# Kernel optimization log

Hardware: AMD Instinct MI355X
Metric: run time of the kernel (lower is better)

Reference implementation:

```python
import jax, jax.numpy as jnp
import numpy as np

SPACE_DIM = 3
D = SPACE_DIM + 1            # (t, x, y, z)
D_MODEL = 1024
N_LAYERS = 4                 # hidden layers
N_MIX = 64
TRI = D * (D - 1) // 2       # strict upper-triangular entries of A
OUT_DIM = N_MIX * (TRI + 1)  # per-mixture triu values + mixture logits
TRIU_I, TRIU_J = np.triu_indices(D, k=1)
RHO_SCALE = 10.0


def setup_inputs() -> dict:
    key = jax.random.key(0)
    ks = jax.random.split(key, 8)
    B = 65536
    x = jax.random.normal(ks[0], (B, D), jnp.float32)
    W0 = jax.random.normal(ks[1], (D, D_MODEL), jnp.float32) * np.float32(np.sqrt(2.0 / D))
    b0 = jnp.zeros((D_MODEL,), jnp.float32)
    Wh = jax.random.normal(ks[2], (N_LAYERS, D_MODEL, D_MODEL), jnp.float32) * np.float32(np.sqrt(2.0 / D_MODEL))
    bh = jnp.zeros((N_LAYERS, D_MODEL), jnp.float32)
    Wout = jax.random.normal(ks[3], (D_MODEL, OUT_DIM), jnp.float32) * np.float32(np.sqrt(1.0 / D_MODEL))
    bout = jnp.zeros((OUT_DIM,), jnp.float32)
    return dict(x=x, W0=W0, b0=b0, Wh=Wh, bh=bh, Wout=Wout, bout=bout)


def _mlp(z, W0, b0, Wh, bh, Wout, bout):
    # z: (D,) -> (OUT_DIM,), swish MLP (NeuralConservationLaw backbone)
    h = jax.nn.silu(z @ W0 + b0)
    for l in range(N_LAYERS):  # fixed small layer count: python loop ok
        h = jax.nn.silu(h @ Wh[l] + bh[l])
    return h @ Wout + bout


def _A(z, params):
    # Antisymmetric matrix field A(z): mixture-weighted strict-upper-tri values.
    out = _mlp(z, *params)                              # (OUT_DIM,)
    logits = out[:N_MIX]                                # (N_MIX,)
    vals = out[N_MIX:].reshape(N_MIX, TRI)              # (N_MIX, TRI)
    a = jax.nn.softmax(logits) @ vals                   # (TRI,)
    A = jnp.zeros((D, D), out.dtype).at[TRIU_I, TRIU_J].set(a)
    return A - A.T                                      # antisymmetric (D, D)


def reference(x, W0, b0, Wh, bh, Wout, bout):
    params = (W0, b0, Wh, bh, Wout, bout)

    def u_single(z):
        # u_i = sum_j dA_ij/dz_j  (row-divergence of antisymmetric A => div u = 0)
        J = jax.jacfwd(lambda zz: _A(zz, params))(z)    # (D, D, D): J[i,j,k]=dA_ij/dz_k
        return jnp.einsum('ijj->i', J)                  # (D,)

    u = jax.vmap(u_single)(x)                           # (B, D)
    rho = u[..., :1] * RHO_SCALE
    flux = u[..., 1:]
    return jnp.concatenate([rho, flux], axis=-1)
```

## Files before the change

### kernel.cpp

```cpp
#include <hip/hip_runtime.h>
#include <hip/hip_bf16.h>

typedef _Float16 half8 __attribute__((ext_vector_type(8)));
typedef _Float16 half4 __attribute__((ext_vector_type(4)));
typedef float floatx4 __attribute__((ext_vector_type(4)));

__device__ __forceinline__ float bfu2f(unsigned short u) {
  return __uint_as_float(((unsigned)u) << 16);
}

__device__ __forceinline__ void gld16(const void* g, void* l) {
  __builtin_amdgcn_global_load_lds((const __attribute__((address_space(1))) void*)g,
                                   (__attribute__((address_space(3))) void*)l, 16, 0, 0);
}

__device__ __forceinline__ float fast_sig(float v) {
  return __builtin_amdgcn_rcpf(1.f + __expf(-v));
}

template <int NC>
__device__ __forceinline__ void xcd_decode(int lin, int NR, int& r, int& c) {
  if (NR & 7) {
    c = lin % NC;
    r = lin / NC;
  } else {
    int rl = lin & 7;
    int t = lin >> 3;
    c = t % NC;
    r = (t / NC) * 8 + rl;
  }
}

__global__ void probe_kernel(const unsigned short* __restrict__ w0, int* __restrict__ flag) {
  __shared__ int s;
  if (threadIdx.x == 0) s = 0;
  __syncthreads();
  int big = 0;
  for (int i = threadIdx.x; i < 2048; i += 256) {
    unsigned e = (w0[i] >> 7) & 0xFFu;
    if (e >= 134u) big = 1;
  }
  if (big) atomicOr(&s, 1);
  __syncthreads();
  if (threadIdx.x == 0) *flag = s;
}

__global__ void cvt_kernel(const void* __restrict__ in, _Float16* __restrict__ out, int nOut,
                           int nIn, const int* __restrict__ flag) {
  int i = blockIdx.x * 256 + threadIdx.x;
  if (i >= nOut) return;
  float v = 0.f;
  if (i < nIn) v = (*flag) ? ((const float*)in)[i] : bfu2f(((const unsigned short*)in)[i]);
  out[i] = (_Float16)v;
}

__global__ void tr_kernel(const void* __restrict__ in, _Float16* __restrict__ out, int Nin,
                          long inStride, long outStride, const int* __restrict__ flag) {
  __shared__ float tile[32][33];
  const int f = *flag;
  int k0 = blockIdx.x * 32, n0 = blockIdx.y * 32;
  long ib = (long)blockIdx.z * inStride;
  long ob = (long)blockIdx.z * outStride;
  int tx = threadIdx.x, ty = threadIdx.y;
#pragma unroll
  for (int i = 0; i < 4; i++) {
    int k = k0 + ty + i * 8, n = n0 + tx;
    float v = 0.f;
    if (n < Nin) {
      long idx = ib + (long)k * Nin + n;
      v = f ? ((const float*)in)[idx] : bfu2f(((const unsigned short*)in)[idx]);
    }
    tile[ty + i * 8][tx] = v;
  }
  __syncthreads();
#pragma unroll
  for (int i = 0; i < 4; i++) {
    int n = n0 + ty + i * 8, k = k0 + tx;
    out[ob + (long)n * 1024 + k] = (_Float16)tile[tx][ty + i * 8];
  }
}

__global__ __launch_bounds__(256)
void layer0_kernel(const _Float16* __restrict__ x16, const _Float16* __restrict__ W0c,
                   const _Float16* __restrict__ b0c, _Float16* __restrict__ H,
                   int chunkBase, int S1) {
  const int lb = blockIdx.x;
  const int t = threadIdx.x;
  const long gb = (long)chunkBase + lb;
  float z0 = (float)x16[gb * 4 + 0];
  float z1 = (float)x16[gb * 4 + 1];
  float z2 = (float)x16[gb * 4 + 2];
  float z3 = (float)x16[gb * 4 + 3];
  const int j0 = t * 4;
  float w[4][4];
#pragma unroll
  for (int i = 0; i < 4; i++) {
    half4 wv = *(const half4*)&W0c[i * 1024 + j0];
#pragma unroll
    for (int jj = 0; jj < 4; jj++) w[i][jj] = (float)wv[jj];
  }
  half4 o[5];
#pragma unroll
  for (int jj = 0; jj < 4; jj++) {
    float pre = z0 * w[0][jj] + z1 * w[1][jj] + z2 * w[2][jj] + z3 * w[3][jj] +
                (float)b0c[j0 + jj];
    float s = fast_sig(pre);
    o[0][jj] = (_Float16)(pre * s);
    float ds = s * (1.f + pre * (1.f - s));
    o[1][jj] = (_Float16)(ds * w[0][jj]);
    o[2][jj] = (_Float16)(ds * w[1][jj]);
    o[3][jj] = (_Float16)(ds * w[2][jj]);
    o[4][jj] = (_Float16)(ds * w[3][jj]);
  }
  long rowbase = (long)lb * 1024 + j0;
#pragma unroll
  for (int s = 0; s < 5; s++) *(half4*)&H[(long)s * S1 + rowbase] = o[s];
}

__global__ __launch_bounds__(256, 3)
void gemm_h1(const _Float16* __restrict__ A, const _Float16* __restrict__ Bt,
             const _Float16* __restrict__ bias, _Float16* __restrict__ C,
             _Float16* __restrict__ DS, int NR) {
  constexpr int K = 1024;
  __shared__ _Float16 SM[8192];
  _Float16* As = SM;
  _Float16* Bs = SM + 4096;
  _Float16* Ep = SM;
  const int tid = threadIdx.x;
  const int wave = tid >> 6;
  const int lane = tid & 63;
  int rb, cb;
  xcd_decode<8>(blockIdx.x, NR, rb, cb);
  const int n0 = cb * 128;
  const long m0 = (long)rb * 128;

  const int srow0 = (wave * 2 + 0) * 16 + (lane >> 2);
  const int srow1 = (wave * 2 + 1) * 16 + (lane >> 2);
  const int scol = (lane & 3) * 8;
  const _Float16* gA0 = A + (m0 + srow0) * K + scol;
  const _Float16* gA1 = A + (m0 + srow1) * K + scol;
  const _Float16* gB0 = Bt + (long)(n0 + srow0) * K + scol;
  const _Float16* gB1 = Bt + (long)(n0 + srow1) * K + scol;
  _Float16* lA0 = As + (wave * 2 + 0) * 512;
  _Float16* lA1 = As + (wave * 2 + 1) * 512;
  _Float16* lB0 = Bs + (wave * 2 + 0) * 512;
  _Float16* lB1 = Bs + (wave * 2 + 1) * 512;

  const int wm = (wave & 1) * 64;
  const int wn = (wave >> 1) * 64;
  const int fr = lane & 15;
  const int fc = (lane >> 4) * 8;
  const int c0f = lane & 15;
  const int rqk = lane >> 4;
  const int myRound = wave & 1;

  float bv[4];
#pragma unroll
  for (int ni = 0; ni < 4; ni++) bv[ni] = (float)bias[n0 + wn + ni * 16 + c0f];

  const int erow = tid >> 4;
  const int ecol = (tid & 15) * 8;
  const int ecolp = ecol ^ (wave << 4);

  floatx4 acc[4][4];
#pragma unroll
  for (int i = 0; i < 4; i++)
#pragma unroll
    for (int j = 0; j < 4; j++) acc[i][j] = (floatx4)(0.f);

  for (int kk = 0; kk < K; kk += 32) {
    __syncthreads();
    gld16(gA0 + kk, lA0);
    gld16(gA1 + kk, lA1);
    gld16(gB0 + kk, lB0);
    gld16(gB1 + kk, lB1);
    __syncthreads();
    half8 af[4], bf[4];
#pragma unroll
    for (int i = 0; i < 4; i++) af[i] = *(const half8*)&As[(wm + i * 16 + fr) * 32 + fc];
#pragma unroll
    for (int i = 0; i < 4; i++) bf[i] = *(const half8*)&Bs[(wn + i * 16 + fr) * 32 + fc];
#pragma unroll
    for (int mi = 0; mi < 4; mi++)
#pragma unroll
      for (int ni = 0; ni < 4; ni++)
        acc[mi][ni] = __builtin_amdgcn_mfma_f32_16x16x32_f16(af[mi], bf[ni], acc[mi][ni], 0, 0, 0);
  }

#pragma unroll
  for (int r = 0; r < 2; r++) {
    __syncthreads();
    if (myRound == r) {
#pragma unroll
      for (int mi = 0; mi < 4; mi++)
#pragma unroll
        for (int ni = 0; ni < 4; ni++) {
          int colp = (wn + ni * 16 + c0f) ^ (rqk << 4);
#pragma unroll
          for (int rr = 0; rr < 4; rr++) {
            int row_local = mi * 16 + rqk * 4 + rr;
            Ep[row_local * 128 + colp] = (_Float16)(acc[mi][ni][rr] + bv[ni]);
          }
        }
    }
    __syncthreads();
#pragma unroll
    for (int p = 0; p < 4; p++) {
      int row_local = p * 16 + erow;
      half8 vv = *(const half8*)&Ep[row_local * 128 + ecolp];
      long row = m0 + r * 64 + row_local;
      half8 hv, dv;
#pragma unroll
      for (int e = 0; e < 8; e++) {
        float xv = (float)vv[e];
        float sg = fast_sig(xv);
        hv[e] = (_Float16)(xv * sg);
        dv[e] = (_Float16)(sg * (1.f + xv * (1.f - sg)));
      }
      *(half8*)&C[row * (long)K + n0 + ecol] = hv;
      *(half8*)&DS[row * (long)K + n0 + ecol] = dv;
    }
  }
}

__global__ __launch_bounds__(512, 2)
void gemm_h2(const _Float16* __restrict__ A, const _Float16* __restrict__ Bt,
             _Float16* __restrict__ C, const _Float16* __restrict__ DS, int bcMask, int NR) {
  constexpr int K = 1024;
  __shared__ _Float16 SM[49152];
  const int tid = threadIdx.x;
  const int wave = tid >> 6;
  const int lane = tid & 63;
  int rb, cb;
  xcd_decode<4>(blockIdx.x, NR, rb, cb);
  const long m0 = (long)rb * 256;
  const int n0 = cb * 256;

  const int srow = wave * 32 + (lane >> 2);
  const int scol = ((lane & 3) ^ ((lane >> 3) & 3)) * 8;
  const _Float16* gA0 = A + (m0 + srow) * K + scol;
  const _Float16* gA1 = gA0 + 16 * K;
  const _Float16* gB0 = Bt + (long)(n0 + srow) * K + scol;
  const _Float16* gB1 = gB0 + 16 * K;
  const int loff0 = wave * 1024;
  const int loff1 = loff0 + 512;

  const int wr = wave >> 2;
  const int wc = wave & 3;
  const int fr = lane & 15;
  const int fc = ((lane >> 4) ^ ((lane >> 1) & 3)) * 8;
  const int rqk = lane >> 4;
  const int c0f = lane & 15;

  floatx4 acc[8][4];
#pragma unroll
  for (int i = 0; i < 8; i++)
#pragma unroll
    for (int j = 0; j < 4; j++) acc[i][j] = (floatx4)(0.f);

  {
    _Float16* b0p = SM;
    gld16(gA0 + 0, b0p + loff0);
    gld16(gA1 + 0, b0p + loff1);
    gld16(gB0 + 0, b0p + 8192 + loff0);
    gld16(gB1 + 0, b0p + 8192 + loff1);
    _Float16* b1p = SM + 16384;
    gld16(gA0 + 32, b1p + loff0);
    gld16(gA1 + 32, b1p + loff1);
    gld16(gB0 + 32, b1p + 8192 + loff0);
    gld16(gB1 + 32, b1p + 8192 + loff1);
  }

  int bufCur = 0;
  int bufNxt = 2;
  for (int it = 0; it < 32; ++it) {
    if (it < 31) __builtin_amdgcn_s_waitcnt(0x0F74);
    else         __builtin_amdgcn_s_waitcnt(0x0F70);
    __builtin_amdgcn_s_barrier();
    const int kk = (it + 2) * 32;
    _Float16* bp = SM + bufNxt * 16384;
    if (it < 30) {
      gld16(gA0 + kk, bp + loff0);
      gld16(gA1 + kk, bp + loff1);
    }
    const _Float16* Asb = SM + bufCur * 16384;
    const _Float16* Bsb = Asb + 8192;
    half8 af[8], bf0, bf1, bf2, bf3;
#pragma unroll
    for (int i = 0; i < 8; i++)
      af[i] = *(const half8*)&Asb[(wr * 128 + i * 16 + fr) * 32 + fc];
    bf0 = *(const half8*)&Bsb[(wc * 64 + 0 * 16 + fr) * 32 + fc];
    bf1 = *(const half8*)&Bsb[(wc * 64 + 1 * 16 + fr) * 32 + fc];
    __builtin_amdgcn_s_setprio(1);
#pragma unroll
    for (int mi = 0; mi < 8; mi++) {
      acc[mi][0] = __builtin_amdgcn_mfma_f32_16x16x32_f16(af[mi], bf0, acc[mi][0], 0, 0, 0);
      acc[mi][1] = __builtin_amdgcn_mfma_f32_16x16x32_f16(af[mi], bf1, acc[mi][1], 0, 0, 0);
    }
    __builtin_amdgcn_s_setprio(0);
    if (it < 30) {
      gld16(gB0 + kk, bp + 8192 + loff0);
      gld16(gB1 + kk, bp + 8192 + loff1);
    }
    bf2 = *(const half8*)&Bsb[(wc * 64 + 2 * 16 + fr) * 32 + fc];
    bf3 = *(const half8*)&Bsb[(wc * 64 + 3 * 16 + fr) * 32 + fc];
    __builtin_amdgcn_s_setprio(1);
#pragma unroll
    for (int mi = 0; mi < 8; mi++) {
      acc[mi][2] = __builtin_amdgcn_mfma_f32_16x16x32_f16(af[mi], bf2, acc[mi][2], 0, 0, 0);
      acc[mi][3] = __builtin_amdgcn_mfma_f32_16x16x32_f16(af[mi], bf3, acc[mi][3], 0, 0, 0);
    }
    __builtin_amdgcn_s_setprio(0);
    bufCur = (bufCur == 2) ? 0 : bufCur + 1;
    bufNxt = (bufNxt == 2) ? 0 : bufNxt + 1;
  }

  const int erow = tid >> 3;
  const int rqkr = (erow >> 2) & 3;
#pragma unroll
  for (int r = 0; r < 4; ++r) {
    __syncthreads();
    if (wr == (r >> 1)) {
      const int mib = (r & 1) * 4;
#pragma unroll
      for (int mi2 = 0; mi2 < 4; ++mi2) {
#pragma unroll
        for (int ni = 0; ni < 4; ++ni) {
          int colp = (wc * 64 + ni * 16 + c0f) ^ (rqk << 4);
#pragma unroll
          for (int rr = 0; rr < 4; ++rr) {
            int row_local = mi2 * 16 + rqk * 4 + rr;
            SM[row_local * 256 + colp] = (_Float16)acc[mib + mi2][ni][rr];
          }
        }
      }
    }
    __syncthreads();
    long grow = m0 + r * 64 + erow;
    long dsrow = grow & bcMask;
#pragma unroll
    for (int q = 0; q < 4; ++q) {
      int col = (tid & 7) * 8 + q * 64;
      int colp = col ^ (rqkr << 4);
      half8 vv = *(const half8*)&SM[erow * 256 + colp];
      half8 dv = *(const half8*)&DS[dsrow * (long)K + n0 + col];
      *(half8*)&C[grow * (long)K + n0 + col] = dv * vv;
    }
  }
}

__global__ __launch_bounds__(256, 4)
void gemm_out(const _Float16* __restrict__ A, const _Float16* __restrict__ Bt,
              const _Float16* __restrict__ bias, _Float16* __restrict__ C,
              int Nreal, int ldc, int biasRows, int NR) {
  constexpr int K = 1024;
  __shared__ _Float16 SM[8192];
  _Float16* As = SM;
  _Float16* Bs = SM + 4096;
  _Float16* Ep = SM;
  const int tid = threadIdx.x;
  const int wave = tid >> 6;
  const int lane = tid & 63;
  int rb, cb;
  xcd_decode<4>(blockIdx.x, NR, rb, cb);
  const int n0 = cb * 128;
  const long m0 = (long)rb * 128;

  const int srow0 = (wave * 2 + 0) * 16 + (lane >> 2);
  const int srow1 = (wave * 2 + 1) * 16 + (lane >> 2);
  const int scol = (lane & 3) * 8;
  const _Float16* gA0 = A + (m0 + srow0) * K + scol;
  const _Float16* gA1 = A + (m0 + srow1) * K + scol;
  const _Float16* gB0 = Bt + (long)(n0 + srow0) * K + scol;
  const _Float16* gB1 = Bt + (long)(n0 + srow1) * K + scol;
  _Float16* lA0 = As + (wave * 2 + 0) * 512;
  _Float16* lA1 = As + (wave * 2 + 1) * 512;
  _Float16* lB0 = Bs + (wave * 2 + 0) * 512;
  _Float16* lB1 = Bs + (wave * 2 + 1) * 512;

  const int wm = (wave & 1) * 64;
  const int wn = (wave >> 1) * 64;
  const int fr = lane & 15;
  const int fc = (lane >> 4) * 8;
  const int c0f = lane & 15;
  const int rqk = lane >> 4;
  const int myRound = wave & 1;

  float bv[4];
#pragma unroll
  for (int ni = 0; ni < 4; ni++) bv[ni] = (float)bias[n0 + wn + ni * 16 + c0f];

  const int erow = tid >> 4;
  const int ecol = (tid & 15) * 8;
  const int ecolp = ecol ^ (wave << 4);

  floatx4 acc[4][4];
#pragma unroll
  for (int i = 0; i < 4; i++)
#pragma unroll
    for (int j = 0; j < 4; j++) acc[i][j] = (floatx4)(0.f);

  for (int kk = 0; kk < K; kk += 32) {
    __syncthreads();
    gld16(gA0 + kk, lA0);
    gld16(gA1 + kk, lA1);
    gld16(gB0 + kk, lB0);
    gld16(gB1 + kk, lB1);
    __syncthreads();
    half8 af[4], bf[4];
#pragma unroll
    for (int i = 0; i < 4; i++) af[i] = *(const half8*)&As[(wm + i * 16 + fr) * 32 + fc];
#pragma unroll
    for (int i = 0; i < 4; i++) bf[i] = *(const half8*)&Bs[(wn + i * 16 + fr) * 32 + fc];
#pragma unroll
    for (int mi = 0; mi < 4; mi++)
#pragma unroll
      for (int ni = 0; ni < 4; ni++)
        acc[mi][ni] = __builtin_amdgcn_mfma_f32_16x16x32_f16(af[mi], bf[ni], acc[mi][ni], 0, 0, 0);
  }

#pragma unroll
  for (int r = 0; r < 2; r++) {
    __syncthreads();
    if (myRound == r) {
#pragma unroll
      for (int mi = 0; mi < 4; mi++)
#pragma unroll
        for (int ni = 0; ni < 4; ni++) {
          int colp = (wn + ni * 16 + c0f) ^ (rqk << 4);
#pragma unroll
          for (int rr = 0; rr < 4; rr++) {
            int row_local = mi * 16 + rqk * 4 + rr;
            long grow = m0 + wm + mi * 16 + rqk * 4 + rr;
            float v = acc[mi][ni][rr] + (grow < biasRows ? bv[ni] : 0.f);
            Ep[row_local * 128 + colp] = (_Float16)v;
          }
        }
    }
    __syncthreads();
#pragma unroll
    for (int p = 0; p < 4; p++) {
      int row_local = p * 16 + erow;
      int col = n0 + ecol;
      if (col < Nreal) {
        half8 vv = *(const half8*)&Ep[row_local * 128 + ecolp];
        long row = m0 + r * 64 + row_local;
        *(half8*)&C[row * (long)ldc + col] = vv;
      }
    }
  }
}

__global__ __launch_bounds__(256)
void finalize_kernel(const _Float16* __restrict__ O5, void* __restrict__ outp,
                     int chunkBase, int Bc, const int* __restrict__ flag) {
  const int wid = threadIdx.x >> 6;
  const int lane = threadIdx.x & 63;
  const int lb = blockIdx.x * 4 + wid;
  const long SO = (long)Bc * 448;
  const long base0 = (long)lb * 448;

  union UU { unsigned u; _Float16 h[2]; };

  float lg = (float)O5[base0 + lane];
  float vals[6];
  {
    const unsigned* vp = (const unsigned*)(O5 + base0 + 64 + lane * 6);
#pragma unroll
    for (int q = 0; q < 3; q++) {
      UU c; c.u = vp[q];
      vals[2 * q] = (float)c.h[0];
      vals[2 * q + 1] = (float)c.h[1];
    }
  }
  float dl[4], dv[4][6];
#pragma unroll
  for (int t = 0; t < 4; t++) {
    long bs = (long)(1 + t) * SO + base0;
    dl[t] = (float)O5[bs + lane];
    const unsigned* vp = (const unsigned*)(O5 + bs + 64 + lane * 6);
#pragma unroll
    for (int q = 0; q < 3; q++) {
      UU c; c.u = vp[q];
      dv[t][2 * q] = (float)c.h[0];
      dv[t][2 * q + 1] = (float)c.h[1];
    }
  }
  float mx = lg;
#pragma unroll
  for (int off = 32; off >= 1; off >>= 1) mx = fmaxf(mx, __shfl_xor(mx, off));
  float e = __expf(lg - mx);
  float S = e;
#pragma unroll
  for (int off = 32; off >= 1; off >>= 1) S += __shfl_xor(S, off);
  float pv = e / S;
  float st[4];
#pragma unroll
  for (int t = 0; t < 4; t++) {
    float v = pv * dl[t];
#pragma unroll
    for (int off = 32; off >= 1; off >>= 1) v += __shfl_xor(v, off);
    st[t] = v;
  }
  float da[4][6];
#pragma unroll
  for (int t = 0; t < 4; t++) {
    float w = pv * (dl[t] - st[t]);
#pragma unroll
    for (int k = 0; k < 6; k++) {
      float v = w * vals[k] + pv * dv[t][k];
#pragma unroll
      for (int off = 32; off >= 1; off >>= 1) v += __shfl_xor(v, off);
      da[t][k] = v;
    }
  }
  if (lane == 0) {
    float u0 = da[1][0] + da[2][1] + da[3][2];
    float u1 = -da[0][0] + da[2][3] + da[3][4];
    float u2 = -da[0][1] - da[1][3] + da[3][5];
    float u3 = -da[0][2] - da[1][4] - da[2][5];
    long ob = (long)(chunkBase + lb) * 4;
    if (*flag) {
      float* o = (float*)outp;
      o[ob] = 10.f * u0; o[ob + 1] = u1; o[ob + 2] = u2; o[ob + 3] = u3;
    } else {
      __hip_bfloat16* o = (__hip_bfloat16*)outp;
      o[ob] = __float2bfloat16(10.f * u0);
      o[ob + 1] = __float2bfloat16(u1);
      o[ob + 2] = __float2bfloat16(u2);
      o[ob + 3] = __float2bfloat16(u3);
    }
  }
}

extern "C" void kernel_launch(void* const* d_in, const int* in_sizes, int n_in,
                              void* d_out, int out_size, void* d_ws, size_t ws_size,
                              hipStream_t stream) {
  const void* x = d_in[0];
  const void* W0 = d_in[1];
  const void* b0 = d_in[2];
  const void* Wh = d_in[3];
  const void* bh = d_in[4];
  const void* Wout = d_in[5];
  const void* bout = d_in[6];
  const int B = in_sizes[0] / 4;

  char* p = (char*)d_ws;
  int* flag = (int*)p;                 p += 256;
  _Float16* W0c = (_Float16*)p;        p += 4096 * 2;
  _Float16* b0c = (_Float16*)p;        p += 1024 * 2;
  _Float16* bhc = (_Float16*)p;        p += 4096 * 2;
  _Float16* boutc = (_Float16*)p;      p += 512 * 2;
  p += 256 - ((size_t)(p - (char*)d_ws) & 255);
  _Float16* x16 = (_Float16*)p;        p += (size_t)B * 4 * 2;
  _Float16* WhT = (_Float16*)p;        p += (size_t)4 * 1024 * 1024 * 2;
  _Float16* WoutT = (_Float16*)p;      p += (size_t)512 * 1024 * 2;
  size_t used = (size_t)(p - (char*)d_ws);
  size_t rem = (ws_size > used) ? (ws_size - used) : 0;
  const size_t perS = 10240 + 10240 + 2048 + 4480;
  long bcap = (long)(rem / perS);
  int Bc = 128;
  while ((long)Bc * 2 <= bcap && Bc * 2 <= B) Bc *= 2;
  _Float16* Ha = (_Float16*)p;         p += (size_t)5 * Bc * 1024 * 2;
  _Float16* Hb = (_Float16*)p;         p += (size_t)5 * Bc * 1024 * 2;
  _Float16* DS = (_Float16*)p;         p += (size_t)Bc * 1024 * 2;
  _Float16* PREo = (_Float16*)p;

  probe_kernel<<<1, 256, 0, stream>>>((const unsigned short*)W0, flag);
  cvt_kernel<<<(B * 4 + 255) / 256, 256, 0, stream>>>(x, x16, B * 4, B * 4, flag);
  cvt_kernel<<<16, 256, 0, stream>>>(W0, W0c, 4096, 4096, flag);
  cvt_kernel<<<4, 256, 0, stream>>>(b0, b0c, 1024, 1024, flag);
  cvt_kernel<<<16, 256, 0, stream>>>(bh, bhc, 4096, 4096, flag);
  cvt_kernel<<<2, 256, 0, stream>>>(bout, boutc, 512, 448, flag);
  tr_kernel<<<dim3(32, 32, 4), dim3(32, 8), 0, stream>>>(Wh, WhT, 1024, 1024L * 1024, 1024L * 1024, flag);
  tr_kernel<<<dim3(32, 16, 1), dim3(32, 8), 0, stream>>>(Wout, WoutT, 448, 0L, 0L, flag);

  const int nChunks = B / Bc;
  for (int c = 0; c < nChunks; c++) {
    const int base = c * Bc;
    const int S1 = Bc * 1024;
    _Float16* Hin = Ha;
    _Float16* Hout = Hb;
    layer0_kernel<<<Bc, 256, 0, stream>>>(x16, W0c, b0c, Hin, base, S1);
    const int NR1 = Bc / 128;
    const int NR2row = Bc / 64;
    const int NRo = 5 * Bc / 128;
    for (int l = 0; l < 4; l++) {
      const _Float16* Wl = WhT + (size_t)l * 1024 * 1024;
      gemm_h1<<<8 * NR1, 256, 0, stream>>>(
          Hin, Wl, bhc + l * 1024, Hout, DS, NR1);
      gemm_h2<<<4 * NR2row, 512, 0, stream>>>(
          Hin + S1, Wl, Hout + S1, DS, Bc - 1, NR2row);
      _Float16* t = Hin; Hin = Hout; Hout = t;
    }
    gemm_out<<<4 * NRo, 256, 0, stream>>>(
        Hin, WoutT, boutc, PREo, 448, 448, Bc, NRo);
    finalize_kernel<<<Bc / 4, 256, 0, stream>>>(PREo, d_out, base, Bc, flag);
  }
}
```

Baseline: 4.178 ms.

## Switch gemm_h2 to double-buffered 64-wide K steps with fewer barriers

Replaces the triple-buffered 32-wide K pipeline in the hidden-layer GEMM with a double-buffered scheme where each stage holds two 32-wide K slices, so the loop runs 16 iterations and issues half as many barriers. Shared memory per block grows from 96KB to 128KB. The goal is to cut synchronisation overhead per K-step, but the larger LDS footprint may lower blocks per CU, and a prefetch issued only one stage ahead may expose load latency.

```diff
diff --git a/kernel.cpp b/kernel.cpp
--- a/kernel.cpp
+++ b/kernel.cpp
@@ -227,7 +227,7 @@
 void gemm_h2(const _Float16* __restrict__ A, const _Float16* __restrict__ Bt,
              _Float16* __restrict__ C, const _Float16* __restrict__ DS, int bcMask, int NR) {
   constexpr int K = 1024;
-  __shared__ _Float16 SM[49152];
+  __shared__ _Float16 SM[65536];
   const int tid = threadIdx.x;
   const int wave = tid >> 6;
   const int lane = tid & 63;
@@ -264,55 +264,56 @@
     gld16(gA1 + 0, b0p + loff1);
     gld16(gB0 + 0, b0p + 8192 + loff0);
     gld16(gB1 + 0, b0p + 8192 + loff1);
-    _Float16* b1p = SM + 16384;
-    gld16(gA0 + 32, b1p + loff0);
-    gld16(gA1 + 32, b1p + loff1);
-    gld16(gB0 + 32, b1p + 8192 + loff0);
-    gld16(gB1 + 32, b1p + 8192 + loff1);
-  }
-
-  int bufCur = 0;
-  int bufNxt = 2;
-  for (int it = 0; it < 32; ++it) {
-    if (it < 31) __builtin_amdgcn_s_waitcnt(0x0F74);
-    else         __builtin_amdgcn_s_waitcnt(0x0F70);
+    gld16(gA0 + 32, b0p + 16384 + loff0);
+    gld16(gA1 + 32, b0p + 16384 + loff1);
+    gld16(gB0 + 32, b0p + 16384 + 8192 + loff0);
+    gld16(gB1 + 32, b0p + 16384 + 8192 + loff1);
+  }
+
+  for (int p = 0; p < 16; ++p) {
     __builtin_amdgcn_s_barrier();
-    const int kk = (it + 2) * 32;
-    _Float16* bp = SM + bufNxt * 16384;
-    if (it < 30) {
+    if (p < 15) {
+      const int kk = (p + 1) * 64;
+      _Float16* bp = SM + ((p + 1) & 1) * 32768;
       gld16(gA0 + kk, bp + loff0);
       gld16(gA1 + kk, bp + loff1);
-    }
-    const _Float16* Asb = SM + bufCur * 16384;
-    const _Float16* Bsb = Asb + 8192;
-    half8 af[8], bf0, bf1, bf2, bf3;
-#pragma unroll
-    for (int i = 0; i < 8; i++)
-      af[i] = *(const half8*)&Asb[(wr * 128 + i * 16 + fr) * 32 + fc];
-    bf0 = *(const half8*)&Bsb[(wc * 64 + 0 * 16 + fr) * 32 + fc];
-    bf1 = *(const half8*)&Bsb[(wc * 64 + 1 * 16 + fr) * 32 + fc];
-    __builtin_amdgcn_s_setprio(1);
-#pragma unroll
-    for (int mi = 0; mi < 8; mi++) {
-      acc[mi][0] = __builtin_amdgcn_mfma_f32_16x16x32_f16(af[mi], bf0, acc[mi][0], 0, 0, 0);
-      acc[mi][1] = __builtin_amdgcn_mfma_f32_16x16x32_f16(af[mi], bf1, acc[mi][1], 0, 0, 0);
-    }
-    __builtin_amdgcn_s_setprio(0);
-    if (it < 30) {
       gld16(gB0 + kk, bp + 8192 + loff0);
       gld16(gB1 + kk, bp + 8192 + loff1);
-    }
-    bf2 = *(const half8*)&Bsb[(wc * 64 + 2 * 16 + fr) * 32 + fc];
-    bf3 = *(const half8*)&Bsb[(wc * 64 + 3 * 16 + fr) * 32 + fc];
-    __builtin_amdgcn_s_setprio(1);
-#pragma unroll
-    for (int mi = 0; mi < 8; mi++) {
-      acc[mi][2] = __builtin_amdgcn_mfma_f32_16x16x32_f16(af[mi], bf2, acc[mi][2], 0, 0, 0);
-      acc[mi][3] = __builtin_amdgcn_mfma_f32_16x16x32_f16(af[mi], bf3, acc[mi][3], 0, 0, 0);
-    }
-    __builtin_amdgcn_s_setprio(0);
-    bufCur = (bufCur == 2) ? 0 : bufCur + 1;
-    bufNxt = (bufNxt == 2) ? 0 : bufNxt + 1;
+      gld16(gA0 + kk + 32, bp + 16384 + loff0);
+      gld16(gA1 + kk + 32, bp + 16384 + loff1);
+      gld16(gB0 + kk + 32, bp + 16384 + 8192 + loff0);
+      gld16(gB1 + kk + 32, bp + 16384 + 8192 + loff1);
+      __builtin_amdgcn_s_waitcnt(0x0F78);
+    } else {
+      __builtin_amdgcn_s_waitcnt(0x0F70);
+    }
+#pragma unroll
+    for (int h = 0; h < 2; ++h) {
+      const _Float16* Asb = SM + (p & 1) * 32768 + h * 16384;
+      const _Float16* Bsb = Asb + 8192;
+      half8 af[8], bf0, bf1, bf2, bf3;
+#pragma unroll
+      for (int i = 0; i < 8; i++)
+        af[i] = *(const half8*)&Asb[(wr * 128 + i * 16 + fr) * 32 + fc];
+      bf0 = *(const half8*)&Bsb[(wc * 64 + 0 * 16 + fr) * 32 + fc];
+      bf1 = *(const half8*)&Bsb[(wc * 64 + 1 * 16 + fr) * 32 + fc];
+      __builtin_amdgcn_s_setprio(1);
+#pragma unroll
+      for (int mi = 0; mi < 8; mi++) {
+        acc[mi][0] = __builtin_amdgcn_mfma_f32_16x16x32_f16(af[mi], bf0, acc[mi][0], 0, 0, 0);
+        acc[mi][1] = __builtin_amdgcn_mfma_f32_16x16x32_f16(af[mi], bf1, acc[mi][1], 0, 0, 0);
+      }
+      __builtin_amdgcn_s_setprio(0);
+      bf2 = *(const half8*)&Bsb[(wc * 64 + 2 * 16 + fr) * 32 + fc];
+      bf3 = *(const half8*)&Bsb[(wc * 64 + 3 * 16 + fr) * 32 + fc];
+      __builtin_amdgcn_s_setprio(1);
+#pragma unroll
+      for (int mi = 0; mi < 8; mi++) {
+        acc[mi][2] = __builtin_amdgcn_mfma_f32_16x16x32_f16(af[mi], bf2, acc[mi][2], 0, 0, 0);
+        acc[mi][3] = __builtin_amdgcn_mfma_f32_16x16x32_f16(af[mi], bf3, acc[mi][3], 0, 0, 0);
+      }
+      __builtin_amdgcn_s_setprio(0);
+    }
   }
 
   const int erow = tid >> 3;
```

After: 4.229 ms. About the same (+1.2%).
